# Optimization experiments

Measured on AMD Instinct MI355X. Metric: run time of the kernel, lower is better.

Reference implementation:

```python
import jax, jax.numpy as jnp
import numpy as np
import math

L, C, H, FF, V, T, B = 12, 768, 12, 3072, 50257, 512, 4
D = C // H  # head dim = 64


def _layernorm(x, w, b, eps=1e-5):
    m = x.mean(-1, keepdims=True)
    v = ((x - m) ** 2).mean(-1, keepdims=True)
    return (x - m) / jnp.sqrt(v + eps) * w + b


def _gelu(x):
    # tanh-approximate GELU exactly as in the torch module
    return 0.5 * x * (1.0 + jnp.tanh(math.sqrt(2.0 / math.pi) * (x + 0.044715 * x ** 3)))


def setup_inputs() -> dict:
    key = jax.random.key(0)
    ks = jax.random.split(key, 12)
    std = 0.02
    proj_std = 0.02 / math.sqrt(2 * L)
    inp = {
        "idx": jax.random.randint(ks[0], (B, T), 0, V),
        "targets": jax.random.randint(ks[1], (B, T), 0, V),
        "wte": jax.random.normal(ks[2], (V, C), jnp.float32) * std,
        "wpe": jax.random.normal(ks[3], (T, C), jnp.float32) * std,
        "ln1_w": jnp.ones((L, C), jnp.float32),
        "ln1_b": jnp.zeros((L, C), jnp.float32),
        "attn_w": jax.random.normal(ks[4], (L, C, 3 * C), jnp.float32) * std,
        "attn_b": jnp.zeros((L, 3 * C), jnp.float32),
        "attnp_w": jax.random.normal(ks[5], (L, C, C), jnp.float32) * proj_std,
        "attnp_b": jnp.zeros((L, C), jnp.float32),
        "ln2_w": jnp.ones((L, C), jnp.float32),
        "ln2_b": jnp.zeros((L, C), jnp.float32),
        "fc_w": jax.random.normal(ks[6], (L, C, FF), jnp.float32) * std,
        "fc_b": jnp.zeros((L, FF), jnp.float32),
        "fcp_w": jax.random.normal(ks[7], (L, FF, C), jnp.float32) * proj_std,
        "fcp_b": jnp.zeros((L, C), jnp.float32),
        "lnf_w": jnp.ones((C,), jnp.float32),
        "lnf_b": jnp.zeros((C,), jnp.float32),
        "lm_w": jax.random.normal(ks[8], (C, V), jnp.float32) * std,  # lm_head.weight.T
    }
    return inp


def _gpt_forward(idx, targets, wte, wpe, ln1_w, ln1_b, attn_w, attn_b,
                 attnp_w, attnp_b, ln2_w, ln2_b, fc_w, fc_b, fcp_w, fcp_b,
                 lnf_w, lnf_b, lm_w):
    b, t = idx.shape
    x = wte[idx] + wpe[:t][None]  # [B,T,C]
    causal = jnp.tril(jnp.ones((t, t), bool))  # [T,T]
    neg_inf = jnp.float32(-jnp.inf)

    def block(x, p):
        l1w, l1b, aw, ab, pw, pb, l2w, l2b, fw, fb, qw, qb = p
        h = _layernorm(x, l1w, l1b)
        qkv = h @ aw + ab  # [B,T,3C]
        q, k, v = jnp.split(qkv, 3, axis=-1)
        q = q.reshape(b, t, H, D).transpose(0, 2, 1, 3)  # [B,H,T,D]
        k = k.reshape(b, t, H, D).transpose(0, 2, 1, 3)
        v = v.reshape(b, t, H, D).transpose(0, 2, 1, 3)
        att = jnp.einsum('bhqd,bhkd->bhqk', q, k) * (1.0 / math.sqrt(D))
        att = jnp.where(causal, att, neg_inf)
        att = jax.nn.softmax(att, axis=-1)
        y = jnp.einsum('bhqk,bhkd->bhqd', att, v)  # [B,H,T,D]
        y = y.transpose(0, 2, 1, 3).reshape(b, t, C)
        x = x + (y @ pw + pb)
        h2 = _layernorm(x, l2w, l2b)
        x = x + (_gelu(h2 @ fw + fb) @ qw + qb)
        return x, None

    params = (ln1_w, ln1_b, attn_w, attn_b, attnp_w, attnp_b,
              ln2_w, ln2_b, fc_w, fc_b, fcp_w, fcp_b)
    x, _ = jax.lax.scan(block, x, params)
    x = _layernorm(x, lnf_w, lnf_b)
    logits = x @ lm_w  # [B,T,V]

    # cross_entropy with ignore_index=-100
    logp = jax.nn.log_softmax(logits, axis=-1)
    tgt = targets.reshape(-1)
    valid = (tgt != -100)
    safe_tgt = jnp.where(valid, tgt, 0)
    nll = -jnp.take_along_axis(logp.reshape(-1, logits.shape[-1]),
                               safe_tgt[:, None], axis=1)[:, 0]
    loss = jnp.sum(nll * valid) / jnp.maximum(jnp.sum(valid), 1)
    return logits, loss


def reference(idx, targets, wte, wpe, ln1_w, ln1_b, attn_w, attn_b,
              attnp_w, attnp_b, ln2_w, ln2_b, fc_w, fc_b, fcp_w, fcp_b,
              lnf_w, lnf_b, lm_w):
    return _gpt_forward(idx, targets, wte, wpe, ln1_w, ln1_b, attn_w, attn_b,
                        attnp_w, attnp_b, ln2_w, ln2_b, fc_w, fc_b,
                        fcp_w, fcp_b, lnf_w, lnf_b, lm_w)
```

## Files before the change

kernel.cpp:

```cpp
#include <hip/hip_runtime.h>
#include <hip/hip_bf16.h>
#include <math.h>

#define L_ 12
#define C_ 768
#define H_ 12
#define FF_ 3072
#define V_ 50257
#define VP2_ 50432
#define T_ 512
#define B_ 4
#define D_ 64
#define M_ (B_*T_)
#define BH_ (B_*H_)
#define NPAN_LM 197

typedef __attribute__((ext_vector_type(8))) short short8;
typedef __attribute__((ext_vector_type(4))) float f32x4;
typedef __attribute__((ext_vector_type(8))) unsigned short us8;
typedef __attribute__((ext_vector_type(4))) unsigned short us4;

__device__ __forceinline__ float bf2f(unsigned short u) {
    return __uint_as_float(((unsigned)u) << 16);
}
__device__ __forceinline__ unsigned short f2bf(float f) {
    unsigned u = __float_as_uint(f);
    unsigned r = u + 0x7fff + ((u >> 16) & 1);
    return (unsigned short)(r >> 16);
}

__device__ __forceinline__ void transpose_tile(
    const float* __restrict__ W, __hip_bfloat16* __restrict__ WT,
    int K, int N, int Npad, int bx, int by, int bz)
{
    __shared__ float tile[64][65];
    const float* Wl = W + (size_t)bz * K * N;
    __hip_bfloat16* WTl = WT + (size_t)bz * Npad * K;
    int k0 = by * 64, n0 = bx * 64;
    int tid = threadIdx.x;
    int tn = tid & 63, tk4 = tid >> 6;
#pragma unroll 4
    for (int i = 0; i < 16; ++i) {
        int k = tk4 * 16 + i;
        int n = n0 + tn;
        tile[k][tn] = (n < N) ? Wl[(size_t)(k0 + k) * N + n] : 0.f;
    }
    __syncthreads();
#pragma unroll
    for (int i = 0; i < 2; ++i) {
        int p = tid + i * 256;
        int n = p >> 3;
        int k8 = (p & 7) * 8;
        us8 v;
#pragma unroll
        for (int e = 0; e < 8; ++e) v[e] = f2bf(tile[k8 + e][n]);
        *(us8*)((unsigned short*)WTl + (size_t)(n0 + n) * K + k0 + k8) = v;
    }
}

__global__ __launch_bounds__(256) void transpose_all_kernel(
    const float* W0, __hip_bfloat16* T0,
    const float* W1, __hip_bfloat16* T1,
    const float* W2, __hip_bfloat16* T2,
    const float* W3, __hip_bfloat16* T3,
    const float* W4, __hip_bfloat16* T4)
{
    int bid = blockIdx.x;
    if (bid < 5184) {
        int bx = bid % 36, r = bid / 36;
        transpose_tile(W0, T0, C_, 3 * C_, 3 * C_, bx, r % 12, r / 12);
    } else if (bid < 6912) {
        int lb = bid - 5184;
        int bx = lb % 12, r = lb / 12;
        transpose_tile(W1, T1, C_, C_, C_, bx, r % 12, r / 12);
    } else if (bid < 13824) {
        int lb = bid - 6912;
        int bx = lb % 48, r = lb / 48;
        transpose_tile(W2, T2, C_, FF_, FF_, bx, r % 12, r / 12);
    } else if (bid < 20736) {
        int lb = bid - 13824;
        int bx = lb % 12, r = lb / 12;
        transpose_tile(W3, T3, FF_, C_, C_, bx, r % 48, r / 48);
    } else {
        int lb = bid - 20736;
        int bx = lb % 788, by = lb / 788;
        transpose_tile(W4, T4, C_, V_, VP2_, bx, by, 0);
    }
}

__global__ __launch_bounds__(256) void embed_kernel(
    const int* __restrict__ idx, const float* __restrict__ wte,
    const float* __restrict__ wpe, float* __restrict__ x, int total4)
{
    int i = blockIdx.x * blockDim.x + threadIdx.x;
    if (i >= total4) return;
    const int CQ = C_ / 4;
    int c4 = (i % CQ) * 4;
    int row = i / CQ;
    int t = row % T_;
    f32x4 a = *(const f32x4*)(wte + (size_t)idx[row] * C_ + c4);
    f32x4 b = *(const f32x4*)(wpe + (size_t)t * C_ + c4);
    *(f32x4*)(x + (size_t)row * C_ + c4) = a + b;
}

__global__ __launch_bounds__(256) void layernorm_kernel(
    const float* __restrict__ x, const float* __restrict__ w, const float* __restrict__ b,
    __hip_bfloat16* __restrict__ out)
{
    int wv = threadIdx.x >> 6, lane = threadIdx.x & 63;
    int row = blockIdx.x * 4 + wv;
    const float* xr = x + (size_t)row * C_;
    f32x4 v[3];
    float s = 0.f;
#pragma unroll
    for (int j = 0; j < 3; ++j) {
        v[j] = *(const f32x4*)(xr + j * 256 + lane * 4);
        s += v[j][0] + v[j][1] + v[j][2] + v[j][3];
    }
#pragma unroll
    for (int off = 32; off; off >>= 1) s += __shfl_xor(s, off, 64);
    float mean = s * (1.f / (float)C_);
    float var = 0.f;
#pragma unroll
    for (int j = 0; j < 3; ++j)
#pragma unroll
        for (int e = 0; e < 4; ++e) { float d = v[j][e] - mean; var += d * d; }
#pragma unroll
    for (int off = 32; off; off >>= 1) var += __shfl_xor(var, off, 64);
    float rstd = rsqrtf(var * (1.f / (float)C_) + 1e-5f);
    unsigned short* o = (unsigned short*)out + (size_t)row * C_;
#pragma unroll
    for (int j = 0; j < 3; ++j) {
        int c0 = j * 256 + lane * 4;
        f32x4 wv4 = *(const f32x4*)(w + c0);
        f32x4 bv4 = *(const f32x4*)(b + c0);
        us4 u;
#pragma unroll
        for (int e = 0; e < 4; ++e)
            u[e] = f2bf((v[j][e] - mean) * rstd * wv4[e] + bv4[e]);
        *(us4*)(o + c0) = u;
    }
}

template<int MT, int NT, int WM, int WN, int BUFS, int SPLITK,
         int OUTBF, int GELU, int RESID, int LOSSP, int QKVPACK, int ATOMIC>
__global__ __launch_bounds__(64 * WM * WN) void mfma_gemm(
    const __hip_bfloat16* __restrict__ A,
    const __hip_bfloat16* __restrict__ Bt,
    const float* __restrict__ bias,
    const float* __restrict__ resid,
    void* __restrict__ Cout,
    int M, int N, int K, int NB,
    float* __restrict__ lpart, int NPAN,
    unsigned short* __restrict__ Qp, unsigned short* __restrict__ Kp,
    unsigned short* __restrict__ Vt)
{
    constexpr int NTHREADS = 64 * WM * WN;
    constexpr int MPAN = M_ / MT;
    constexpr int MFR = MT / (16 * WM);
    constexpr int AL = (MT * 4) / NTHREADS;
    constexpr int BL = (NT * 4) / NTHREADS;
    constexpr int LOADS = AL + BL;

    int nwg = NB * MPAN * SPLITK;
    int orig = blockIdx.x;
    int xcd = orig & 7;
    int q = nwg >> 3, rr_ = nwg & 7;
    int wgid = (xcd < rr_ ? xcd * (q + 1) : rr_ * (q + 1) + (xcd - rr_) * q) + (orig >> 3);
    int chunk = wgid / (NB * MPAN);
    int rem = wgid % (NB * MPAN);
    int npan = rem / MPAN, mpan = rem % MPAN;
    int m0 = mpan * MT, n0 = npan * NT;
    int KC = K / SPLITK;
    int kbase = chunk * KC;

    __shared__ __hip_bfloat16 As[BUFS][MT * 32];
    __shared__ __hip_bfloat16 Bs[BUFS][NT * 32];
    __shared__ float Lsum[WN][LOSSP ? MT : 1];
    int tid = threadIdx.x;
    int lane = tid & 63, w = tid >> 6;
    int wn = w % WN, wm = w / WN;
    int lrow = lane & 15, g = lane >> 4;
    f32x4 acc[MFR][4] = {};

    const __hip_bfloat16* Ab = A + (size_t)m0 * K + kbase;
    const __hip_bfloat16* Bb = Bt + (size_t)n0 * K + kbase;

    auto stage = [&](int buf, int k0) {
#pragma unroll
        for (int i = 0; i < AL; ++i) {
            int c = tid + i * NTHREADS;
            int row = c >> 2, s = c & 3;
            int l = (s - (row >> 1)) & 3;
            __builtin_amdgcn_global_load_lds(
                (const __attribute__((address_space(1))) void*)(Ab + (size_t)row * K + k0 + l * 8),
                (__attribute__((address_space(3))) void*)(&As[buf][c * 8]), 16, 0, 0);
        }
#pragma unroll
        for (int i = 0; i < BL; ++i) {
            int c = tid + i * NTHREADS;
            int row = c >> 2, s = c & 3;
            int l = (s - (row >> 1)) & 3;
            __builtin_amdgcn_global_load_lds(
                (const __attribute__((address_space(1))) void*)(Bb + (size_t)row * K + k0 + l * 8),
                (__attribute__((address_space(3))) void*)(&Bs[buf][c * 8]), 16, 0, 0);
        }
    };
    auto do_tile = [&](int buf) {
        short8 a[MFR], b[4];
#pragma unroll
        for (int i = 0; i < MFR; ++i) {
            int row = wm * (MT / WM) + i * 16 + lrow;
            int s = (g + (row >> 1)) & 3;
            a[i] = *(const short8*)&As[buf][row * 32 + s * 8];
        }
#pragma unroll
        for (int j = 0; j < 4; ++j) {
            int row = wn * 64 + j * 16 + lrow;
            int s = (g + (row >> 1)) & 3;
            b[j] = *(const short8*)&Bs[buf][row * 32 + s * 8];
        }
        asm volatile("s_waitcnt lgkmcnt(0)" ::: "memory");
        __builtin_amdgcn_sched_barrier(0);
        __builtin_amdgcn_s_setprio(1);
#pragma unroll
        for (int i = 0; i < MFR; ++i)
#pragma unroll
            for (int j = 0; j < 4; ++j)
                acc[i][j] = __builtin_amdgcn_mfma_f32_16x16x32_bf16(a[i], b[j], acc[i][j], 0, 0, 0);
        __builtin_amdgcn_s_setprio(0);
    };

    int nk = KC >> 5;
#pragma unroll
    for (int i = 0; i < BUFS - 1; ++i) stage(i, i << 5);
    for (int t = 0; t < nk; ++t) {
        int ahead = nk - 1 - t;
        if (ahead > BUFS - 2) ahead = BUFS - 2;
        if (ahead == 1) {
            if constexpr (LOADS == 3) asm volatile("s_waitcnt vmcnt(3)" ::: "memory");
            else                      asm volatile("s_waitcnt vmcnt(4)" ::: "memory");
        } else if (ahead >= 2) {
            if constexpr (LOADS == 3) asm volatile("s_waitcnt vmcnt(6)" ::: "memory");
            else                      asm volatile("s_waitcnt vmcnt(8)" ::: "memory");
        } else {
            asm volatile("s_waitcnt vmcnt(0)" ::: "memory");
        }
        __builtin_amdgcn_s_barrier();
        if (t + BUFS - 1 < nk) stage((t + BUFS - 1) % BUFS, (t + BUFS - 1) << 5);
        do_tile(t % BUFS);
    }

    int r0 = g * 4;
    if (QKVPACK) {
        int which = n0 / 768;
#pragma unroll
        for (int i = 0; i < MFR; ++i) {
#pragma unroll
            for (int j = 0; j < 4; ++j) {
                int col = n0 + wn * 64 + j * 16 + lrow;
                float bv = bias ? bias[col] : 0.f;
                int cc = col - which * 768;
                int hh = cc >> 6, d = cc & 63;
                int row0 = m0 + wm * (MT / WM) + i * 16 + r0;
                int bb = row0 >> 9, tt0 = row0 & (T_ - 1);
                size_t bh = (size_t)bb * H_ + hh;
                if (which == 2) {
                    us4 u;
#pragma unroll
                    for (int r = 0; r < 4; ++r) u[r] = f2bf(acc[i][j][r] + bv);
                    *(us4*)(Vt + (bh * 64 + d) * T_ + tt0) = u;
                } else {
                    unsigned short* dst = (which == 0) ? Qp : Kp;
#pragma unroll
                    for (int r = 0; r < 4; ++r)
                        dst[(bh * T_ + tt0 + r) * 64 + d] = f2bf(acc[i][j][r] + bv);
                }
            }
        }
    } else {
#pragma unroll
        for (int i = 0; i < MFR; ++i) {
#pragma unroll
            for (int j = 0; j < 4; ++j) {
                int col = n0 + wn * 64 + j * 16 + lrow;
                if (col >= N) continue;
                float bv = (bias && (SPLITK == 1 || chunk == 0)) ? bias[col] : 0.f;
#pragma unroll
                for (int r = 0; r < 4; ++r) {
                    int row = m0 + wm * (MT / WM) + i * 16 + r0 + r;
                    float v = acc[i][j][r] + bv;
                    if (GELU) {
                        float t = 0.7978845608028654f * (v + 0.044715f * v * v * v);
                        v = 0.5f * v * (1.f + tanhf(t));
                    }
                    if (RESID) v += resid[(size_t)row * N + col];
                    if (ATOMIC) {
                        atomicAdd(&((float*)Cout)[(size_t)row * N + col], v);
                    } else if (OUTBF) {
                        ((unsigned short*)Cout)[(size_t)row * N + col] = f2bf(v);
                    } else {
                        ((float*)Cout)[(size_t)row * N + col] = v;
                    }
                }
            }
        }
    }
    if (LOSSP) {
#pragma unroll
        for (int i = 0; i < MFR; ++i) {
#pragma unroll
            for (int r = 0; r < 4; ++r) {
                float ss = 0.f;
#pragma unroll
                for (int j = 0; j < 4; ++j) {
                    int col = n0 + wn * 64 + j * 16 + lrow;
                    if (col < V_) ss += __expf(acc[i][j][r]);
                }
#pragma unroll
                for (int d2 = 1; d2 < 16; d2 <<= 1) ss += __shfl_xor(ss, d2, 64);
                if ((lane & 15) == 0) {
                    int rloc = wm * (MT / WM) + i * 16 + g * 4 + r;
                    Lsum[wn][rloc] = ss;
                }
            }
        }
        __syncthreads();
        if (tid < MT) {
            float ss = Lsum[0][tid];
#pragma unroll
            for (int ww = 1; ww < WN; ++ww) ss += Lsum[ww][tid];
            lpart[(size_t)(m0 + tid) * NPAN + npan] = ss;
        }
    }
}

__global__ __launch_bounds__(256) void flash_attn_kernel(
    const unsigned short* __restrict__ Qp, const unsigned short* __restrict__ Kp,
    const unsigned short* __restrict__ Vt, unsigned short* __restrict__ y)
{
    int bid = blockIdx.x;
    int xcd = bid & 7;
    int s_ = bid >> 3;
    int bh = xcd * 6 + (s_ % 6);
    int qg = 7 - s_ / 6;
    int b = bh / H_, h = bh % H_;
    int tid = threadIdx.x;
    int w = tid >> 6;
    int lane = tid & 63;
    int c = lane & 15, g = lane >> 4;
    int q0 = (qg * 4 + w) * 16;

    const unsigned short* Qb = Qp + ((size_t)bh * T_ + q0) * 64;
    const unsigned short* Kb = Kp + (size_t)bh * T_ * 64;
    const unsigned short* Vb = Vt + (size_t)bh * 64 * T_;

    short8 qf0 = *(const short8*)(Qb + (size_t)c * 64 + g * 8);
    short8 qf1 = *(const short8*)(Qb + (size_t)c * 64 + 32 + g * 8);

    f32x4 o[4] = {};
    float mrow[4], lrow[4];
#pragma unroll
    for (int r = 0; r < 4; ++r) { mrow[r] = -1e30f; lrow[r] = 0.f; }

    __shared__ unsigned short P_lds[4][16 * 40];

    auto qk_tile = [&](int kv0, f32x4& t0, f32x4& t1) {
        t0 = (f32x4){0.f, 0.f, 0.f, 0.f};
        t1 = (f32x4){0.f, 0.f, 0.f, 0.f};
        const unsigned short* Kt0 = Kb + (size_t)(kv0 + c) * 64;
        short8 b0 = *(const short8*)(Kt0 + g * 8);
        short8 b1 = *(const short8*)(Kt0 + 32 + g * 8);
        const unsigned short* Kt1 = Kb + (size_t)(kv0 + 16 + c) * 64;
        short8 b2 = *(const short8*)(Kt1 + g * 8);
        short8 b3 = *(const short8*)(Kt1 + 32 + g * 8);
        __builtin_amdgcn_s_setprio(1);
        t0 = __builtin_amdgcn_mfma_f32_16x16x32_bf16(qf0, b0, t0, 0, 0, 0);
        t0 = __builtin_amdgcn_mfma_f32_16x16x32_bf16(qf1, b1, t0, 0, 0, 0);
        t1 = __builtin_amdgcn_mfma_f32_16x16x32_bf16(qf0, b2, t1, 0, 0, 0);
        t1 = __builtin_amdgcn_mfma_f32_16x16x32_bf16(qf1, b3, t1, 0, 0, 0);
        __builtin_amdgcn_s_setprio(0);
    };

    int ntiles = q0 / 32 + 1;
    f32x4 sN0, sN1;
    qk_tile(0, sN0, sN1);
    for (int t = 0; t < ntiles; ++t) {
        int kv0 = t * 32;
        f32x4 s0 = sN0, s1 = sN1;
        if (t + 1 < ntiles) qk_tile(kv0 + 32, sN0, sN1);
        if (kv0 + 32 > q0) {
#pragma unroll
            for (int r = 0; r < 4; ++r) {
                int qq = q0 + g * 4 + r;
                float v0 = s0[r] * 0.125f;
                float v1 = s1[r] * 0.125f;
                s0[r] = (kv0 + c <= qq) ? v0 : -1e30f;
                s1[r] = (kv0 + 16 + c <= qq) ? v1 : -1e30f;
            }
        } else {
#pragma unroll
            for (int r = 0; r < 4; ++r) { s0[r] *= 0.125f; s1[r] *= 0.125f; }
        }
        float pmax[4];
#pragma unroll
        for (int r = 0; r < 4; ++r) pmax[r] = fmaxf(s0[r], s1[r]);
#pragma unroll
        for (int d2 = 1; d2 < 16; d2 <<= 1)
#pragma unroll
            for (int r = 0; r < 4; ++r) pmax[r] = fmaxf(pmax[r], __shfl_xor(pmax[r], d2, 64));
        float scl[4], psum[4];
#pragma unroll
        for (int r = 0; r < 4; ++r) {
            float mnew = fmaxf(mrow[r], pmax[r]);
            scl[r] = __expf(mrow[r] - mnew);
            mrow[r] = mnew;
            s0[r] = __expf(s0[r] - mnew);
            s1[r] = __expf(s1[r] - mnew);
            psum[r] = s0[r] + s1[r];
        }
#pragma unroll
        for (int d2 = 1; d2 < 16; d2 <<= 1)
#pragma unroll
            for (int r = 0; r < 4; ++r) psum[r] += __shfl_xor(psum[r], d2, 64);
#pragma unroll
        for (int r = 0; r < 4; ++r) lrow[r] = lrow[r] * scl[r] + psum[r];
#pragma unroll
        for (int j = 0; j < 4; ++j)
#pragma unroll
            for (int r = 0; r < 4; ++r) o[j][r] *= scl[r];
#pragma unroll
        for (int r = 0; r < 4; ++r) {
            P_lds[w][(g * 4 + r) * 40 + c] = f2bf(s0[r]);
            P_lds[w][(g * 4 + r) * 40 + 16 + c] = f2bf(s1[r]);
        }
        asm volatile("s_waitcnt lgkmcnt(0)" ::: "memory");
        __builtin_amdgcn_sched_barrier(0);
        short8 pf = *(const short8*)&P_lds[w][c * 40 + g * 8];
        asm volatile("s_waitcnt lgkmcnt(0)" ::: "memory");
        asm volatile("" ::: "memory");
        __builtin_amdgcn_s_setprio(1);
#pragma unroll
        for (int j = 0; j < 4; ++j) {
            short8 vf = *(const short8*)(Vb + (size_t)(j * 16 + c) * T_ + kv0 + g * 8);
            o[j] = __builtin_amdgcn_mfma_f32_16x16x32_bf16(pf, vf, o[j], 0, 0, 0);
        }
        __builtin_amdgcn_s_setprio(0);
    }
    unsigned short* yb = y + ((size_t)(b * T_ + q0)) * C_ + h * 64;
#pragma unroll
    for (int r = 0; r < 4; ++r) {
        float inv = 1.f / lrow[r];
#pragma unroll
        for (int j = 0; j < 4; ++j)
            yb[(size_t)(g * 4 + r) * C_ + j * 16 + c] = f2bf(o[j][r] * inv);
    }
}

__global__ __launch_bounds__(256) void loss_reduce_kernel(
    const float* __restrict__ lpart, const float* __restrict__ logits,
    const int* __restrict__ targets, float* __restrict__ rnll, int NPAN)
{
    int row = blockIdx.x;
    const float* pp = lpart + (size_t)row * NPAN;
    int tid = threadIdx.x;
    float s = 0.f;
    for (int j = tid; j < NPAN; j += 256) s += pp[j];
    for (int off = 32; off > 0; off >>= 1) s += __shfl_down(s, off, 64);
    __shared__ float rs[4];
    if ((tid & 63) == 0) rs[tid >> 6] = s;
    __syncthreads();
    if (tid == 0) {
        float S = rs[0] + rs[1] + rs[2] + rs[3];
        int t = targets[row];
        if (t != -100) {
            rnll[row] = -(logits[(size_t)row * V_ + t] - logf(S));
            rnll[M_ + row] = 1.f;
        } else {
            rnll[row] = 0.f;
            rnll[M_ + row] = 0.f;
        }
    }
}

__global__ __launch_bounds__(256) void finalize_loss(
    const float* __restrict__ rnll, float* __restrict__ out)
{
    int tid = threadIdx.x;
    float sn = 0.f, sc = 0.f;
    for (int j = tid; j < M_; j += 256) { sn += rnll[j]; sc += rnll[M_ + j]; }
    for (int off = 32; off > 0; off >>= 1) {
        sn += __shfl_down(sn, off, 64);
        sc += __shfl_down(sc, off, 64);
    }
    __shared__ float rn[4], rc[4];
    if ((tid & 63) == 0) { rn[tid >> 6] = sn; rc[tid >> 6] = sc; }
    __syncthreads();
    if (tid == 0) {
        float N = rn[0] + rn[1] + rn[2] + rn[3];
        float Cn = rc[0] + rc[1] + rc[2] + rc[3];
        out[0] = N / fmaxf(Cn, 1.f);
    }
}

extern "C" void kernel_launch(void* const* d_in, const int* in_sizes, int n_in,
                              void* d_out, int out_size, void* d_ws, size_t ws_size,
                              hipStream_t stream)
{
    const int*   idx     = (const int*)d_in[0];
    const int*   targets = (const int*)d_in[1];
    const float* wte     = (const float*)d_in[2];
    const float* wpe     = (const float*)d_in[3];
    const float* ln1_w   = (const float*)d_in[4];
    const float* ln1_b   = (const float*)d_in[5];
    const float* attn_w  = (const float*)d_in[6];
    const float* attn_b  = (const float*)d_in[7];
    const float* attnp_w = (const float*)d_in[8];
    const float* attnp_b = (const float*)d_in[9];
    const float* ln2_w   = (const float*)d_in[10];
    const float* ln2_b   = (const float*)d_in[11];
    const float* fc_w    = (const float*)d_in[12];
    const float* fc_b    = (const float*)d_in[13];
    const float* fcp_w   = (const float*)d_in[14];
    const float* fcp_b   = (const float*)d_in[15];
    const float* lnf_w   = (const float*)d_in[16];
    const float* lnf_b   = (const float*)d_in[17];
    const float* lm_w    = (const float*)d_in[18];

    float* logits = (float*)d_out;
    float* loss   = logits + (size_t)M_ * V_;

    char* p = (char*)d_ws;
    __hip_bfloat16* aw_t = (__hip_bfloat16*)p; p += (size_t)L_ * 3 * C_ * C_ * 2;
    __hip_bfloat16* pw_t = (__hip_bfloat16*)p; p += (size_t)L_ * C_ * C_ * 2;
    __hip_bfloat16* fw_t = (__hip_bfloat16*)p; p += (size_t)L_ * FF_ * C_ * 2;
    __hip_bfloat16* qw_t = (__hip_bfloat16*)p; p += (size_t)L_ * C_ * FF_ * 2;
    __hip_bfloat16* lm_t = (__hip_bfloat16*)p; p += (size_t)VP2_ * C_ * 2;
    float*          x    = (float*)p;          p += (size_t)M_ * C_ * 4;
    __hip_bfloat16* h    = (__hip_bfloat16*)p; p += (size_t)M_ * C_ * 2;
    __hip_bfloat16* y    = (__hip_bfloat16*)p; p += (size_t)M_ * C_ * 2;
    __hip_bfloat16* ff   = (__hip_bfloat16*)p; p += (size_t)M_ * FF_ * 2;
    unsigned short* Qp   = (unsigned short*)p; p += (size_t)BH_ * T_ * 64 * 2;
    unsigned short* Kp   = (unsigned short*)p; p += (size_t)BH_ * T_ * 64 * 2;
    unsigned short* Vt   = (unsigned short*)p; p += (size_t)BH_ * 64 * T_ * 2;
    float*          lpart= (float*)p;          p += (size_t)M_ * NPAN_LM * 4;
    float*          rnll = (float*)p;          p += (size_t)2 * M_ * 4;

    transpose_all_kernel<<<30192, 256, 0, stream>>>(
        attn_w, aw_t, attnp_w, pw_t, fc_w, fw_t, fcp_w, qw_t, lm_w, lm_t);

    {
        int total4 = M_ * C_ / 4;
        embed_kernel<<<(total4 + 255) / 256, 256, 0, stream>>>(idx, wte, wpe, x, total4);
    }

    for (int l = 0; l < L_; ++l) {
        const float* l1w = ln1_w + (size_t)l * C_;
        const float* l1b = ln1_b + (size_t)l * C_;
        const __hip_bfloat16* aw = aw_t + (size_t)l * 3 * C_ * C_;
        const float* ab  = attn_b + (size_t)l * 3 * C_;
        const __hip_bfloat16* pw = pw_t + (size_t)l * C_ * C_;
        const float* pb  = attnp_b + (size_t)l * C_;
        const float* l2w = ln2_w + (size_t)l * C_;
        const float* l2b = ln2_b + (size_t)l * C_;
        const __hip_bfloat16* fw = fw_t + (size_t)l * FF_ * C_;
        const float* fb  = fc_b + (size_t)l * FF_;
        const __hip_bfloat16* qw = qw_t + (size_t)l * C_ * FF_;
        const float* qb  = fcp_b + (size_t)l * C_;

        layernorm_kernel<<<M_ / 4, 256, 0, stream>>>(x, l1w, l1b, h);
        mfma_gemm<64, 128, 2, 2, 2, 1, 0, 0, 0, 0, 1, 0><<<18 * 32, 256, 0, stream>>>(
            h, aw, ab, nullptr, nullptr, M_, 3 * C_, C_, 18, nullptr, 0, Qp, Kp, Vt);
        flash_attn_kernel<<<384, 256, 0, stream>>>(Qp, Kp, Vt, (unsigned short*)y);
        mfma_gemm<64, 128, 2, 2, 2, 2, 0, 0, 0, 0, 0, 1><<<6 * 32 * 2, 256, 0, stream>>>(
            y, pw, pb, nullptr, x, M_, C_, C_, 6, nullptr, 0, nullptr, nullptr, nullptr);
        layernorm_kernel<<<M_ / 4, 256, 0, stream>>>(x, l2w, l2b, h);
        mfma_gemm<64, 128, 2, 2, 2, 1, 1, 1, 0, 0, 0, 0><<<24 * 32, 256, 0, stream>>>(
            h, fw, fb, nullptr, ff, M_, FF_, C_, 24, nullptr, 0, nullptr, nullptr, nullptr);
        mfma_gemm<64, 128, 2, 2, 2, 4, 0, 0, 0, 0, 0, 1><<<6 * 32 * 4, 256, 0, stream>>>(
            ff, qw, qb, nullptr, x, M_, C_, FF_, 6, nullptr, 0, nullptr, nullptr, nullptr);
    }

    layernorm_kernel<<<M_ / 4, 256, 0, stream>>>(x, lnf_w, lnf_b, h);
    mfma_gemm<128, 256, 2, 4, 2, 1, 0, 0, 0, 1, 0, 0><<<NPAN_LM * 16, 512, 0, stream>>>(
        h, lm_t, nullptr, nullptr, logits, M_, V_, C_, NPAN_LM, lpart, NPAN_LM,
        nullptr, nullptr, nullptr);

    loss_reduce_kernel<<<M_, 256, 0, stream>>>(lpart, logits, targets, rnll, NPAN_LM);
    finalize_loss<<<1, 256, 0, stream>>>(rnll, loss);
}
```

Baseline: 2.197 ms.

## Repack LM-head logits through shared memory for coalesced stores; triple-buffer GEMMs

Adds a REPACK epilogue to the LM-head GEMM. The accumulator tile is staged through shared memory in two halves, so each wave writes full contiguous 64-float row segments of the large fp32 logits tensor and computes the per-row exp partial sums in the same pass. This targets the scattered 4-byte stores of the old fragment-layout epilogue on the output that dominates traffic. Separately, every GEMM moves from 2 to 3 LDS pipeline buffers, which increases shared memory per block and may reduce occupancy.

```diff
diff --git a/kernel.cpp b/kernel.cpp
--- a/kernel.cpp
+++ b/kernel.cpp
@@ -143,7 +143,7 @@
 }
 
 template<int MT, int NT, int WM, int WN, int BUFS, int SPLITK,
-         int OUTBF, int GELU, int RESID, int LOSSP, int QKVPACK, int ATOMIC>
+         int OUTBF, int GELU, int RESID, int LOSSP, int QKVPACK, int ATOMIC, int REPACK>
 __global__ __launch_bounds__(64 * WM * WN) void mfma_gemm(
     const __hip_bfloat16* __restrict__ A,
     const __hip_bfloat16* __restrict__ Bt,
@@ -161,6 +161,10 @@
     constexpr int AL = (MT * 4) / NTHREADS;
     constexpr int BL = (NT * 4) / NTHREADS;
     constexpr int LOADS = AL + BL;
+    constexpr int SMEM_STAGE = BUFS * (MT + NT) * 32 * 2;
+    constexpr int SMEM_LS = (LOSSP && !REPACK) ? WN * MT * 4 : 4;
+    constexpr int SMEM_RPK = REPACK ? 64 * 264 * 4 : 0;
+    constexpr int SMEM_TOT = (SMEM_STAGE + SMEM_LS) > SMEM_RPK ? (SMEM_STAGE + SMEM_LS) : SMEM_RPK;
 
     int nwg = NB * MPAN * SPLITK;
     int orig = blockIdx.x;
@@ -174,9 +178,11 @@
     int KC = K / SPLITK;
     int kbase = chunk * KC;
 
-    __shared__ __hip_bfloat16 As[BUFS][MT * 32];
-    __shared__ __hip_bfloat16 Bs[BUFS][NT * 32];
-    __shared__ float Lsum[WN][LOSSP ? MT : 1];
+    __shared__ char smem[SMEM_TOT];
+    __hip_bfloat16* AsB = (__hip_bfloat16*)smem;
+    __hip_bfloat16* BsB = (__hip_bfloat16*)(smem + BUFS * MT * 32 * 2);
+    float* Lsum = (float*)(smem + SMEM_STAGE);
+    float* tileF = (float*)smem;
     int tid = threadIdx.x;
     int lane = tid & 63, w = tid >> 6;
     int wn = w % WN, wm = w / WN;
@@ -194,7 +200,7 @@
             int l = (s - (row >> 1)) & 3;
             __builtin_amdgcn_global_load_lds(
                 (const __attribute__((address_space(1))) void*)(Ab + (size_t)row * K + k0 + l * 8),
-                (__attribute__((address_space(3))) void*)(&As[buf][c * 8]), 16, 0, 0);
+                (__attribute__((address_space(3))) void*)(&AsB[buf * MT * 32 + c * 8]), 16, 0, 0);
         }
 #pragma unroll
         for (int i = 0; i < BL; ++i) {
@@ -203,7 +209,7 @@
             int l = (s - (row >> 1)) & 3;
             __builtin_amdgcn_global_load_lds(
                 (const __attribute__((address_space(1))) void*)(Bb + (size_t)row * K + k0 + l * 8),
-                (__attribute__((address_space(3))) void*)(&Bs[buf][c * 8]), 16, 0, 0);
+                (__attribute__((address_space(3))) void*)(&BsB[buf * NT * 32 + c * 8]), 16, 0, 0);
         }
     };
     auto do_tile = [&](int buf) {
@@ -212,13 +218,13 @@
         for (int i = 0; i < MFR; ++i) {
             int row = wm * (MT / WM) + i * 16 + lrow;
             int s = (g + (row >> 1)) & 3;
-            a[i] = *(const short8*)&As[buf][row * 32 + s * 8];
+            a[i] = *(const short8*)&AsB[buf * MT * 32 + row * 32 + s * 8];
         }
 #pragma unroll
         for (int j = 0; j < 4; ++j) {
             int row = wn * 64 + j * 16 + lrow;
             int s = (g + (row >> 1)) & 3;
-            b[j] = *(const short8*)&Bs[buf][row * 32 + s * 8];
+            b[j] = *(const short8*)&BsB[buf * NT * 32 + row * 32 + s * 8];
         }
         asm volatile("s_waitcnt lgkmcnt(0)" ::: "memory");
         __builtin_amdgcn_sched_barrier(0);
@@ -252,6 +258,44 @@
     }
 
     int r0 = g * 4;
+    if constexpr (REPACK) {
+        float* logitsF = (float*)Cout;
+        __syncthreads();
+#pragma unroll
+        for (int half = 0; half < 2; ++half) {
+            if (wm == half) {
+#pragma unroll
+                for (int i = 0; i < MFR; ++i)
+#pragma unroll
+                    for (int j = 0; j < 4; ++j)
+#pragma unroll
+                        for (int r = 0; r < 4; ++r)
+                            tileF[(i * 16 + r0 + r) * 264 + wn * 64 + j * 16 + lrow] = acc[i][j][r];
+            }
+            __syncthreads();
+#pragma unroll
+            for (int it = 0; it < 64 / (NTHREADS / 64); ++it) {
+                int rw = it * (NTHREADS / 64) + (tid >> 6);
+                int grow = m0 + half * 64 + rw;
+                float ss = 0.f;
+#pragma unroll
+                for (int e = 0; e < 4; ++e) {
+                    int cl = (tid & 63) + e * 64;
+                    float v = tileF[rw * 264 + cl];
+                    int gcol = n0 + cl;
+                    if (gcol < V_) {
+                        logitsF[(size_t)grow * V_ + gcol] = v;
+                        ss += __expf(v);
+                    }
+                }
+#pragma unroll
+                for (int d2 = 1; d2 < 64; d2 <<= 1) ss += __shfl_xor(ss, d2, 64);
+                if ((tid & 63) == 0) lpart[(size_t)grow * NPAN + npan] = ss;
+            }
+            __syncthreads();
+        }
+        return;
+    }
     if (QKVPACK) {
         int which = n0 / 768;
 #pragma unroll
@@ -306,7 +350,7 @@
             }
         }
     }
-    if (LOSSP) {
+    if constexpr (LOSSP && !REPACK) {
 #pragma unroll
         for (int i = 0; i < MFR; ++i) {
 #pragma unroll
@@ -321,15 +365,15 @@
                 for (int d2 = 1; d2 < 16; d2 <<= 1) ss += __shfl_xor(ss, d2, 64);
                 if ((lane & 15) == 0) {
                     int rloc = wm * (MT / WM) + i * 16 + g * 4 + r;
-                    Lsum[wn][rloc] = ss;
+                    Lsum[wn * MT + rloc] = ss;
                 }
             }
         }
         __syncthreads();
         if (tid < MT) {
-            float ss = Lsum[0][tid];
-#pragma unroll
-            for (int ww = 1; ww < WN; ++ww) ss += Lsum[ww][tid];
+            float ss = Lsum[tid];
+#pragma unroll
+            for (int ww = 1; ww < WN; ++ww) ss += Lsum[ww * MT + tid];
             lpart[(size_t)(m0 + tid) * NPAN + npan] = ss;
         }
     }
@@ -569,20 +613,20 @@
         const float* qb  = fcp_b + (size_t)l * C_;
 
         layernorm_kernel<<<M_ / 4, 256, 0, stream>>>(x, l1w, l1b, h);
-        mfma_gemm<64, 128, 2, 2, 2, 1, 0, 0, 0, 0, 1, 0><<<18 * 32, 256, 0, stream>>>(
+        mfma_gemm<64, 128, 2, 2, 3, 1, 0, 0, 0, 0, 1, 0, 0><<<18 * 32, 256, 0, stream>>>(
             h, aw, ab, nullptr, nullptr, M_, 3 * C_, C_, 18, nullptr, 0, Qp, Kp, Vt);
         flash_attn_kernel<<<384, 256, 0, stream>>>(Qp, Kp, Vt, (unsigned short*)y);
-        mfma_gemm<64, 128, 2, 2, 2, 2, 0, 0, 0, 0, 0, 1><<<6 * 32 * 2, 256, 0, stream>>>(
+        mfma_gemm<64, 128, 2, 2, 3, 2, 0, 0, 0, 0, 0, 1, 0><<<6 * 32 * 2, 256, 0, stream>>>(
             y, pw, pb, nullptr, x, M_, C_, C_, 6, nullptr, 0, nullptr, nullptr, nullptr);
         layernorm_kernel<<<M_ / 4, 256, 0, stream>>>(x, l2w, l2b, h);
-        mfma_gemm<64, 128, 2, 2, 2, 1, 1, 1, 0, 0, 0, 0><<<24 * 32, 256, 0, stream>>>(
+        mfma_gemm<64, 128, 2, 2, 3, 1, 1, 1, 0, 0, 0, 0, 0><<<24 * 32, 256, 0, stream>>>(
             h, fw, fb, nullptr, ff, M_, FF_, C_, 24, nullptr, 0, nullptr, nullptr, nullptr);
-        mfma_gemm<64, 128, 2, 2, 2, 4, 0, 0, 0, 0, 0, 1><<<6 * 32 * 4, 256, 0, stream>>>(
+        mfma_gemm<64, 128, 2, 2, 3, 4, 0, 0, 0, 0, 0, 1, 0><<<6 * 32 * 4, 256, 0, stream>>>(
             ff, qw, qb, nullptr, x, M_, C_, FF_, 6, nullptr, 0, nullptr, nullptr, nullptr);
     }
 
     layernorm_kernel<<<M_ / 4, 256, 0, stream>>>(x, lnf_w, lnf_b, h);
-    mfma_gemm<128, 256, 2, 4, 2, 1, 0, 0, 0, 1, 0, 0><<<NPAN_LM * 16, 512, 0, stream>>>(
+    mfma_gemm<128, 256, 2, 4, 3, 1, 0, 0, 0, 1, 0, 0, 1><<<NPAN_LM * 16, 512, 0, stream>>>(
         h, lm_t, nullptr, nullptr, logits, M_, V_, C_, NPAN_LM, lpart, NPAN_LM,
         nullptr, nullptr, nullptr);
 
```

Result: faster. 2.081 ms (-5.3%).
